# Performance work log

Measured on AMD Instinct MI355X. Metric: run time of the kernel, lower is better.

The kernel has to match this reference:

```python
import jax, jax.numpy as jnp
import numpy as np

INVALID_TOKEN_ID = -1


def setup_inputs() -> dict:
    key = jax.random.key(0)
    k1, k2 = jax.random.split(key)
    batch, spec_len, vocab = 128, 7, 128000
    total_tokens = batch * (spec_len + 1)
    logits = jax.random.normal(k1, (total_tokens, vocab), dtype=jnp.float32)
    spec_token_ids = jax.random.randint(k2, (batch, spec_len), 0, vocab, dtype=jnp.int64)
    return {"logits": logits, "spec_token_ids": spec_token_ids}


def reference(logits, spec_token_ids):
    # greedy_sample_ref with uniform spec lengths: pad_sequence is a no-op reshape.
    B, k = spec_token_ids.shape  # k = spec_len, each row samples k+1 tokens
    out = jnp.argmax(logits, axis=-1).reshape(B, k + 1)  # [B, k+1] int
    # accept draft token i only if all tokens 0..i matched the target argmax
    accept = jnp.cumprod((out[:, :-1] == spec_token_ids).astype(jnp.int32), axis=1)
    gen = jnp.concatenate([accept.astype(bool), jnp.zeros((B, 1), dtype=bool)], axis=1)
    # also emit the first rejected/bonus position (first zero in gen mask)
    zeros_mask = ~gen
    first_zero = jnp.argmax(zeros_mask.astype(jnp.int32), axis=1)  # [B]
    rows_with_zero = zeros_mask.any(axis=1)  # [B]
    pos = jnp.arange(k + 1)[None, :]
    gen = gen | ((pos == first_zero[:, None]) & rows_with_zero[:, None])
    return jnp.where(gen, out, INVALID_TOKEN_ID)
```

## Files before the change

### kernel.cpp

```cpp
#include <hip/hip_runtime.h>

#define INVALID_TOKEN_ID -1

__device__ __forceinline__ void upd4(float4 v, int base, float& best, int& bestIdx) {
    if (v.x > best) { best = v.x; bestIdx = base; }
    if (v.y > best) { best = v.y; bestIdx = base + 1; }
    if (v.z > best) { best = v.z; bestIdx = base + 2; }
    if (v.w > best) { best = v.w; bestIdx = base + 3; }
}

__global__ __launch_bounds__(512, 8) void rowargmax_kernel(
    const float* __restrict__ logits, int* __restrict__ amax, int vocab) {
    const int row = blockIdx.x;
    const int t = threadIdx.x;
    const float* rowp = logits + (size_t)row * (size_t)vocab;

    const int nvec = vocab >> 2;
    const float4* rowv = (const float4*)rowp;

    float best = -__builtin_inff();
    int idx = 0;

    int i = t;
    for (; i + 3584 < nvec; i += 4096) {
        float4 v0 = rowv[i];
        float4 v1 = rowv[i + 512];
        float4 v2 = rowv[i + 1024];
        float4 v3 = rowv[i + 1536];
        float4 v4 = rowv[i + 2048];
        float4 v5 = rowv[i + 2560];
        float4 v6 = rowv[i + 3072];
        float4 v7 = rowv[i + 3584];
        const int base = i << 2;
        upd4(v0, base, best, idx);
        upd4(v1, base + 2048, best, idx);
        upd4(v2, base + 4096, best, idx);
        upd4(v3, base + 6144, best, idx);
        upd4(v4, base + 8192, best, idx);
        upd4(v5, base + 10240, best, idx);
        upd4(v6, base + 12288, best, idx);
        upd4(v7, base + 14336, best, idx);
    }
    for (; i + 512 < nvec; i += 1024) {
        float4 a = rowv[i];
        float4 b = rowv[i + 512];
        upd4(a, i << 2, best, idx);
        upd4(b, (i + 512) << 2, best, idx);
    }
    if (i < nvec) {
        float4 a = rowv[i];
        upd4(a, i << 2, best, idx);
    }
    for (int j = (nvec << 2) + t; j < vocab; j += 512) {
        float v = rowp[j];
        if (v > best) { best = v; idx = j; }
    }

    #pragma unroll
    for (int off = 32; off > 0; off >>= 1) {
        float ov = __shfl_down(best, off, 64);
        int oi = __shfl_down(idx, off, 64);
        if (ov > best || (ov == best && oi < idx)) { best = ov; idx = oi; }
    }

    __shared__ float svals[8];
    __shared__ int sidx[8];
    const int wave = t >> 6;
    if ((t & 63) == 0) { svals[wave] = best; sidx[wave] = idx; }
    __syncthreads();
    if (t == 0) {
        #pragma unroll
        for (int w = 1; w < 8; ++w) {
            if (svals[w] > best || (svals[w] == best && sidx[w] < idx)) {
                best = svals[w]; idx = sidx[w];
            }
        }
        amax[row] = idx;
    }
}

__global__ void finalize_kernel(const int* __restrict__ amax,
                                const int* __restrict__ spec,
                                int* __restrict__ out, int B, int k) {
    int b = blockIdx.x * blockDim.x + threadIdx.x;
    if (b >= B) return;
    const int kp1 = k + 1;

    int outv[8];
    int gen[8];
    #pragma unroll
    for (int j = 0; j < 8; ++j) { outv[j] = 0; gen[j] = 0; }

    for (int j = 0; j < kp1; ++j) outv[j] = amax[b * kp1 + j];

    int acc = 1;
    int firstZero = k;
    for (int j = 0; j < k; ++j) {
        if (acc && outv[j] != spec[b * k + j]) { acc = 0; firstZero = j; }
        gen[j] = acc;
    }
    gen[k] = 0;
    gen[firstZero] = 1;

    for (int j = 0; j < kp1; ++j)
        out[b * kp1 + j] = gen[j] ? outv[j] : INVALID_TOKEN_ID;
}

extern "C" void kernel_launch(void* const* d_in, const int* in_sizes, int n_in,
                              void* d_out, int out_size, void* d_ws, size_t ws_size,
                              hipStream_t stream) {
    const float* logits = (const float*)d_in[0];
    const int* spec = (const int*)d_in[1];
    int* out = (int*)d_out;

    const int total_tokens = out_size;
    const int vocab = in_sizes[0] / total_tokens;
    const int B = out_size - in_sizes[1];
    const int k = in_sizes[1] / B;

    int* amax = (int*)d_ws;

    rowargmax_kernel<<<total_tokens, 512, 0, stream>>>(logits, amax, vocab);
    finalize_kernel<<<(B + 127) / 128, 128, 0, stream>>>(amax, spec, out, B, k);
}
```

Baseline: 670.5 us.

## Split each row argmax across multiple blocks with nontemporal loads

Each logits row is now split into four segments, each handled by a 256-thread block that writes a partial max value and index. The finalize kernel merges the partials with lowest-index tie-breaking. Loads become nontemporal vector loads with a 4-way unroll instead of 8. The aim is more, smaller blocks for better load balance and memory-level parallelism on a purely bandwidth-bound scan, at the cost of extra partial-result traffic and a slightly longer finalize step.

New measurement: 636.2 us. -5.1%, faster.

```diff
diff --git a/kernel.cpp b/kernel.cpp
--- a/kernel.cpp
+++ b/kernel.cpp
@@ -2,58 +2,52 @@
 
 #define INVALID_TOKEN_ID -1
 
-__device__ __forceinline__ void upd4(float4 v, int base, float& best, int& bestIdx) {
-    if (v.x > best) { best = v.x; bestIdx = base; }
-    if (v.y > best) { best = v.y; bestIdx = base + 1; }
-    if (v.z > best) { best = v.z; bestIdx = base + 2; }
-    if (v.w > best) { best = v.w; bestIdx = base + 3; }
+typedef float f32x4 __attribute__((ext_vector_type(4)));
+
+__device__ __forceinline__ void upd4(f32x4 v, int base, float& best, int& bestIdx) {
+    if (v[0] > best) { best = v[0]; bestIdx = base; }
+    if (v[1] > best) { best = v[1]; bestIdx = base + 1; }
+    if (v[2] > best) { best = v[2]; bestIdx = base + 2; }
+    if (v[3] > best) { best = v[3]; bestIdx = base + 3; }
 }
 
-__global__ __launch_bounds__(512, 8) void rowargmax_kernel(
-    const float* __restrict__ logits, int* __restrict__ amax, int vocab) {
-    const int row = blockIdx.x;
+__global__ __launch_bounds__(256, 4) void rowargmax_part(
+    const float* __restrict__ logits, float* __restrict__ pval,
+    int* __restrict__ pidx, int vocab, int segs) {
+    const int row = blockIdx.x / segs;
+    const int seg = blockIdx.x - row * segs;
     const int t = threadIdx.x;
+
     const float* rowp = logits + (size_t)row * (size_t)vocab;
-
+    const f32x4* rowv = (const f32x4*)rowp;
     const int nvec = vocab >> 2;
-    const float4* rowv = (const float4*)rowp;
+    const int segLen = (nvec + segs - 1) / segs;
+    const int begin = seg * segLen;
+    const int end = min(begin + segLen, nvec);
 
     float best = -__builtin_inff();
     int idx = 0;
 
-    int i = t;
-    for (; i + 3584 < nvec; i += 4096) {
-        float4 v0 = rowv[i];
-        float4 v1 = rowv[i + 512];
-        float4 v2 = rowv[i + 1024];
-        float4 v3 = rowv[i + 1536];
-        float4 v4 = rowv[i + 2048];
-        float4 v5 = rowv[i + 2560];
-        float4 v6 = rowv[i + 3072];
-        float4 v7 = rowv[i + 3584];
-        const int base = i << 2;
-        upd4(v0, base, best, idx);
-        upd4(v1, base + 2048, best, idx);
-        upd4(v2, base + 4096, best, idx);
-        upd4(v3, base + 6144, best, idx);
-        upd4(v4, base + 8192, best, idx);
-        upd4(v5, base + 10240, best, idx);
-        upd4(v6, base + 12288, best, idx);
-        upd4(v7, base + 14336, best, idx);
+    int i = begin + t;
+    for (; i + 768 < end; i += 1024) {
+        f32x4 a = __builtin_nontemporal_load(&rowv[i]);
+        f32x4 b = __builtin_nontemporal_load(&rowv[i + 256]);
+        f32x4 c = __builtin_nontemporal_load(&rowv[i + 512]);
+        f32x4 d = __builtin_nontemporal_load(&rowv[i + 768]);
+        upd4(a, i << 2, best, idx);
+        upd4(b, (i + 256) << 2, best, idx);
+        upd4(c, (i + 512) << 2, best, idx);
+        upd4(d, (i + 768) << 2, best, idx);
     }
-    for (; i + 512 < nvec; i += 1024) {
-        float4 a = rowv[i];
-        float4 b = rowv[i + 512];
-        upd4(a, i << 2, best, idx);
-        upd4(b, (i + 512) << 2, best, idx);
-    }
-    if (i < nvec) {
-        float4 a = rowv[i];
+    for (; i < end; i += 256) {
+        f32x4 a = __builtin_nontemporal_load(&rowv[i]);
         upd4(a, i << 2, best, idx);
     }
-    for (int j = (nvec << 2) + t; j < vocab; j += 512) {
-        float v = rowp[j];
-        if (v > best) { best = v; idx = j; }
+    if (seg == segs - 1) {
+        for (int j = (nvec << 2) + t; j < vocab; j += 256) {
+            float v = rowp[j];
+            if (v > best) { best = v; idx = j; }
+        }
     }
 
     #pragma unroll
@@ -63,25 +57,28 @@
         if (ov > best || (ov == best && oi < idx)) { best = ov; idx = oi; }
     }
 
-    __shared__ float svals[8];
-    __shared__ int sidx[8];
+    __shared__ float svals[4];
+    __shared__ int sidx[4];
     const int wave = t >> 6;
     if ((t & 63) == 0) { svals[wave] = best; sidx[wave] = idx; }
     __syncthreads();
     if (t == 0) {
         #pragma unroll
-        for (int w = 1; w < 8; ++w) {
+        for (int w = 1; w < 4; ++w) {
             if (svals[w] > best || (svals[w] == best && sidx[w] < idx)) {
                 best = svals[w]; idx = sidx[w];
             }
         }
-        amax[row] = idx;
+        const int p = row * segs + seg;
+        pval[p] = best;
+        pidx[p] = idx;
     }
 }
 
-__global__ void finalize_kernel(const int* __restrict__ amax,
+__global__ void finalize_kernel(const float* __restrict__ pval,
+                                const int* __restrict__ pidx,
                                 const int* __restrict__ spec,
-                                int* __restrict__ out, int B, int k) {
+                                int* __restrict__ out, int B, int k, int segs) {
     int b = blockIdx.x * blockDim.x + threadIdx.x;
     if (b >= B) return;
     const int kp1 = k + 1;
@@ -91,7 +88,17 @@
     #pragma unroll
     for (int j = 0; j < 8; ++j) { outv[j] = 0; gen[j] = 0; }
 
-    for (int j = 0; j < kp1; ++j) outv[j] = amax[b * kp1 + j];
+    for (int j = 0; j < kp1; ++j) {
+        const int tok = b * kp1 + j;
+        float bv = pval[tok * segs];
+        int bi = pidx[tok * segs];
+        for (int s = 1; s < segs; ++s) {
+            float v = pval[tok * segs + s];
+            int ix = pidx[tok * segs + s];
+            if (v > bv || (v == bv && ix < bi)) { bv = v; bi = ix; }
+        }
+        outv[j] = bi;
+    }
 
     int acc = 1;
     int firstZero = k;
@@ -118,8 +125,10 @@
     const int B = out_size - in_sizes[1];
     const int k = in_sizes[1] / B;
 
-    int* amax = (int*)d_ws;
+    const int SEGS = 4;
+    float* pval = (float*)d_ws;
+    int* pidx = (int*)(pval + total_tokens * SEGS);
 
-    rowargmax_kernel<<<total_tokens, 512, 0, stream>>>(logits, amax, vocab);
-    finalize_kernel<<<(B + 127) / 128, 128, 0, stream>>>(amax, spec, out, B, k);
+    rowargmax_part<<<total_tokens * SEGS, 256, 0, stream>>>(logits, pval, pidx, vocab, SEGS);
+    finalize_kernel<<<(B + 127) / 128, 128, 0, stream>>>(pval, pidx, spec, out, B, k, SEGS);
 }
```
